# Performance work log

Measured on AMD Instinct MI355X. Metric: run time of the kernel, lower is better.

## Reference

```python
import jax, jax.numpy as jnp
import numpy as np

D_IN, H, H1, H2 = 50, 64, 32, 1

def setup_inputs() -> dict:
    key = jax.random.key(0)
    ks = jax.random.split(key, 13)
    s = 1.0 / np.sqrt(H)
    u = lambda k, shp: jax.random.uniform(k, shp, jnp.float32, -s, s)
    x = jax.random.normal(ks[0], (512, 2048, D_IN), jnp.float32)
    return {
        "x": x,
        "W_ih0": u(ks[1], (H, D_IN)), "W_hh0": u(ks[2], (H, H)),
        "b_ih0": u(ks[3], (H,)),      "b_hh0": u(ks[4], (H,)),
        "W_ih1": u(ks[5], (H, H)),    "W_hh1": u(ks[6], (H, H)),
        "b_ih1": u(ks[7], (H,)),      "b_hh1": u(ks[8], (H,)),
        "W1": u(ks[9], (H1, H)),      "b1": u(ks[10], (H1,)),
        "W2": u(ks[11], (H2, H1)),    "b2": u(ks[12], (H2,)),
    }

def reference(x, W_ih0, W_hh0, b_ih0, b_hh0, W_ih1, W_hh1, b_ih1, b_hh1, W1, b1, W2, b2):
    B = x.shape[0]
    # Precompute input projections for layer 0 for all timesteps: [S, B, H]
    xt = jnp.swapaxes(x, 0, 1)  # [S, B, D_IN]
    x_proj0 = jnp.einsum('sbd,hd->sbh', xt, W_ih0) + b_ih0 + b_hh0

    h0 = jnp.zeros((B, H), x.dtype)

    def step(carry, xp):
        h1, h2 = carry
        h1 = jnp.tanh(xp + h1 @ W_hh0.T)
        h2 = jnp.tanh(h1 @ W_ih1.T + b_ih1 + h2 @ W_hh1.T + b_hh1)
        return (h1, h2), None

    (h1f, h2f), _ = jax.lax.scan(step, (h0, h0), x_proj0)
    hidden = jax.nn.relu(h2f @ W1.T + b1)
    return jax.nn.sigmoid(hidden @ W2.T + b2)
```

## Files before the change

### kernel.cpp

```cpp
#include <hip/hip_runtime.h>

#define S_LEN 2048
#define DIN   50
#define H     64

__device__ __forceinline__ float tanh_fast(float v) {
    float e = __builtin_amdgcn_exp2f(v * 2.885390082f);
    return 1.0f - 2.0f * __builtin_amdgcn_rcpf(e + 1.0f);
}

__device__ __forceinline__ float sum4groups(float v) {
#if __has_builtin(__builtin_amdgcn_permlane16_swap) && __has_builtin(__builtin_amdgcn_permlane32_swap)
    typedef unsigned u2 __attribute__((ext_vector_type(2)));
    u2 r = __builtin_amdgcn_permlane16_swap(__float_as_uint(v), __float_as_uint(v), false, false);
    float s = __uint_as_float(r[0]) + __uint_as_float(r[1]);
    u2 t = __builtin_amdgcn_permlane32_swap(__float_as_uint(s), __float_as_uint(s), false, false);
    return __uint_as_float(t[0]) + __uint_as_float(t[1]);
#else
    v += __shfl_xor(v, 16, 64);
    v += __shfl_xor(v, 32, 64);
    return v;
#endif
}

__global__ __launch_bounds__(256)
__attribute__((amdgpu_waves_per_eu(2, 2)))
void rnn_fused(const float* __restrict__ x,
               const float* __restrict__ W_ih0, const float* __restrict__ W_hh0,
               const float* __restrict__ b_ih0, const float* __restrict__ b_hh0,
               const float* __restrict__ W_ih1, const float* __restrict__ W_hh1,
               const float* __restrict__ b_ih1, const float* __restrict__ b_hh1,
               const float* __restrict__ W1, const float* __restrict__ b1,
               const float* __restrict__ W2, const float* __restrict__ b2,
               float* __restrict__ out)
{
    const int b    = blockIdx.x;
    const int tid  = threadIdx.x;
    const int lane = tid & 63;
    const int w    = tid >> 6;
    const int j    = lane & 15;
    const int kg   = lane >> 4;
    const int outj = 16 * w + j;

    __shared__ __align__(16) float xs[2][4][16];
    __shared__ __align__(16) float h1s[H];
    __shared__ __align__(16) float h2s[H];

    float wx[13];
    #pragma unroll
    for (int i = 0; i < 13; ++i) {
        int c = 13 * kg + i;
        wx[i] = (c < DIN) ? W_ih0[outj * DIN + c] : 0.0f;
    }
    float whh0_l[16], wih1_l[16], whh1_l[16];
    #pragma unroll
    for (int i = 0; i < 16; ++i) {
        whh0_l[i] = W_hh0[outj * H + 16 * kg + i];
        wih1_l[i] = W_ih1[outj * H + 16 * kg + i];
        whh1_l[i] = W_hh1[outj * H + 16 * kg + i];
    }
    const float bias0 = b_ih0[outj] + b_hh0[outj];
    const float bias1 = b_ih1[outj] + b_hh1[outj];

    const float* __restrict__ xrow = x + (size_t)b * (size_t)(S_LEN * DIN);

    const int  sw   = tid >> 4, sj = tid & 15;
    const int  scol = 13 * sw + sj;
    const bool sval = (tid < 64) && (sj < 13) && (scol < DIN);

    if (tid < 64) xs[0][sw][sj] = sval ? xrow[scol] : 0.0f;
    float pfA = sval ? xrow[1 * DIN + scol] : 0.0f;
    float pfB = sval ? xrow[2 * DIN + scol] : 0.0f;
    const float* xpf = xrow + 3 * DIN + scol;

    float h1c[16], h2c[16];
    #pragma unroll
    for (int i = 0; i < 16; ++i) { h1c[i] = 0.0f; h2c[i] = 0.0f; }

    __syncthreads();

    float xacc;
    {
        float a0 = 0, a1 = 0, a2 = 0, a3 = 0;
        #pragma unroll
        for (int q = 0; q < 3; ++q) {
            float4 xv = *(const float4*)&xs[0][kg][4 * q];
            a0 = fmaf(xv.x, wx[4 * q + 0], a0);
            a1 = fmaf(xv.y, wx[4 * q + 1], a1);
            a2 = fmaf(xv.z, wx[4 * q + 2], a2);
            a3 = fmaf(xv.w, wx[4 * q + 3], a3);
        }
        a0 = fmaf(xs[0][kg][12], wx[12], a0);
        xacc = (a0 + a1) + (a2 + a3);
    }

#define STEP_BODY(CUR, NXT, PFOK)                                              \
    {                                                                          \
                  \
        float a0 = xacc, a1 = 0, a2 = 0, a3 = 0;                               \
        _Pragma("unroll")                                                      \
        for (int q = 0; q < 4; ++q) {                                          \
            a0 = fmaf(h1c[4 * q + 0], whh0_l[4 * q + 0], a0);                  \
            a1 = fmaf(h1c[4 * q + 1], whh0_l[4 * q + 1], a1);                  \
            a2 = fmaf(h1c[4 * q + 2], whh0_l[4 * q + 2], a2);                  \
            a3 = fmaf(h1c[4 * q + 3], whh0_l[4 * q + 3], a3);                  \
        }                                                                      \
        float h1n = tanh_fast(sum4groups((a0 + a1) + (a2 + a3)) + bias0);      \
                               \
        if (tid < 64) xs[NXT][sw][sj] = pfA;                                   \
        pfA = pfB;                                                             \
        pfB = (sval && (PFOK)) ? *xpf : 0.0f;                                  \
        xpf += DIN;                                                            \
                          \
        float c0 = 0, c1 = 0, c2 = 0, c3 = 0;                                  \
        _Pragma("unroll")                                                      \
        for (int q = 0; q < 4; ++q) {                                          \
            c0 = fmaf(h2c[4 * q + 0], whh1_l[4 * q + 0], c0);                  \
            c1 = fmaf(h2c[4 * q + 1], whh1_l[4 * q + 1], c1);                  \
            c2 = fmaf(h2c[4 * q + 2], whh1_l[4 * q + 2], c2);                  \
            c3 = fmaf(h2c[4 * q + 3], whh1_l[4 * q + 3], c3);                  \
        }                                                                      \
        if (kg == 0) h1s[16 * w + j] = h1n;                                    \
        __syncthreads();                    \
                    \
        _Pragma("unroll")                                                      \
        for (int q = 0; q < 4; ++q)                                            \
            *(float4*)&h1c[4 * q] = *(const float4*)&h1s[16 * kg + 4 * q];     \
                \
        float xn0 = 0, xn1 = 0, xn2 = 0, xn3 = 0;                              \
        _Pragma("unroll")                                                      \
        for (int q = 0; q < 3; ++q) {                                          \
            float4 xv = *(const float4*)&xs[NXT][kg][4 * q];                   \
            xn0 = fmaf(xv.x, wx[4 * q + 0], xn0);                              \
            xn1 = fmaf(xv.y, wx[4 * q + 1], xn1);                              \
            xn2 = fmaf(xv.z, wx[4 * q + 2], xn2);                              \
            xn3 = fmaf(xv.w, wx[4 * q + 3], xn3);                              \
        }                                                                      \
        xn0 = fmaf(xs[NXT][kg][12], wx[12], xn0);                              \
                                            \
        _Pragma("unroll")                                                      \
        for (int q = 0; q < 4; ++q) {                                          \
            c0 = fmaf(h1c[4 * q + 0], wih1_l[4 * q + 0], c0);                  \
            c1 = fmaf(h1c[4 * q + 1], wih1_l[4 * q + 1], c1);                  \
            c2 = fmaf(h1c[4 * q + 2], wih1_l[4 * q + 2], c2);                  \
            c3 = fmaf(h1c[4 * q + 3], wih1_l[4 * q + 3], c3);                  \
        }                                                                      \
        float h2n = tanh_fast(sum4groups((c0 + c1) + (c2 + c3)) + bias1);      \
        if (kg == 0) h2s[16 * w + j] = h2n;                                    \
        __syncthreads();                               \
        _Pragma("unroll")                                                      \
        for (int q = 0; q < 4; ++q)                                            \
            *(float4*)&h2c[4 * q] = *(const float4*)&h2s[16 * kg + 4 * q];     \
        xacc = (xn0 + xn1) + (xn2 + xn3);                                      \
    }

    for (int s = 0; s < S_LEN; s += 2) {
        STEP_BODY(0, 1, s + 3 < S_LEN)
        STEP_BODY(1, 0, s + 4 < S_LEN)
    }
#undef STEP_BODY

    if (tid < 64) {
        float hv = 0.0f;
        if (lane < 32) {
            float acc = b1[lane];
            #pragma unroll
            for (int k = 0; k < H; ++k)
                acc = fmaf(h2s[k], W1[lane * H + k], acc);
            hv = fmaxf(acc, 0.0f) * W2[lane];
        }
        #pragma unroll
        for (int off = 32; off; off >>= 1)
            hv += __shfl_xor(hv, off, 64);
        if (lane == 0)
            out[b] = 1.0f / (1.0f + __expf(-(hv + b2[0])));
    }
}

extern "C" void kernel_launch(void* const* d_in, const int* in_sizes, int n_in,
                              void* d_out, int out_size, void* d_ws, size_t ws_size,
                              hipStream_t stream) {
    const float* x     = (const float*)d_in[0];
    const float* W_ih0 = (const float*)d_in[1];
    const float* W_hh0 = (const float*)d_in[2];
    const float* b_ih0 = (const float*)d_in[3];
    const float* b_hh0 = (const float*)d_in[4];
    const float* W_ih1 = (const float*)d_in[5];
    const float* W_hh1 = (const float*)d_in[6];
    const float* b_ih1 = (const float*)d_in[7];
    const float* b_hh1 = (const float*)d_in[8];
    const float* W1    = (const float*)d_in[9];
    const float* b1    = (const float*)d_in[10];
    const float* W2    = (const float*)d_in[11];
    const float* b2    = (const float*)d_in[12];
    float* out = (float*)d_out;

    rnn_fused<<<dim3(512), dim3(256), 0, stream>>>(
        x, W_ih0, W_hh0, b_ih0, b_hh0,
        W_ih1, W_hh1, b_ih1, b_hh1,
        W1, b1, W2, b2, out);
}
```

Baseline: 1.064 ms.

## Split each RNN block over eight waves with an eight-way reduction

Doubles the threads per sequence block from 256 to 512, so each wave owns 8 hidden units instead of 16. The reduction dimension is now split into 8 lane groups of 8 elements, so each thread holds half as many weights and does half as many FMAs per step. A DPP row-rotate add is added in front of the existing permlane reduction. The intent is to shorten per-thread work on the serial recurrence and raise wave occupancy, at the cost of an extra reduction stage and barriers that must synchronise twice as many waves every timestep.

```diff
diff --git a/kernel.cpp b/kernel.cpp
--- a/kernel.cpp
+++ b/kernel.cpp
@@ -9,13 +9,20 @@
     return 1.0f - 2.0f * __builtin_amdgcn_rcpf(e + 1.0f);
 }
 
-__device__ __forceinline__ float sum4groups(float v) {
+__device__ __forceinline__ float red8(float v) {
+#if __has_builtin(__builtin_amdgcn_update_dpp)
+    float t = __uint_as_float((unsigned)__builtin_amdgcn_update_dpp(
+        0, (int)__float_as_uint(v), 0x128 , 0xF, 0xF, true));
+    v += t;
+#else
+    v += __shfl_xor(v, 8, 64);
+#endif
 #if __has_builtin(__builtin_amdgcn_permlane16_swap) && __has_builtin(__builtin_amdgcn_permlane32_swap)
     typedef unsigned u2 __attribute__((ext_vector_type(2)));
     u2 r = __builtin_amdgcn_permlane16_swap(__float_as_uint(v), __float_as_uint(v), false, false);
     float s = __uint_as_float(r[0]) + __uint_as_float(r[1]);
-    u2 t = __builtin_amdgcn_permlane32_swap(__float_as_uint(s), __float_as_uint(s), false, false);
-    return __uint_as_float(t[0]) + __uint_as_float(t[1]);
+    u2 q = __builtin_amdgcn_permlane32_swap(__float_as_uint(s), __float_as_uint(s), false, false);
+    return __uint_as_float(q[0]) + __uint_as_float(q[1]);
 #else
     v += __shfl_xor(v, 16, 64);
     v += __shfl_xor(v, 32, 64);
@@ -23,8 +30,8 @@
 #endif
 }
 
-__global__ __launch_bounds__(256)
-__attribute__((amdgpu_waves_per_eu(2, 2)))
+__global__ __launch_bounds__(512)
+__attribute__((amdgpu_waves_per_eu(4, 4)))
 void rnn_fused(const float* __restrict__ x,
                const float* __restrict__ W_ih0, const float* __restrict__ W_hh0,
                const float* __restrict__ b_ih0, const float* __restrict__ b_hh0,
@@ -38,120 +45,105 @@
     const int tid  = threadIdx.x;
     const int lane = tid & 63;
     const int w    = tid >> 6;
-    const int j    = lane & 15;
-    const int kg   = lane >> 4;
-    const int outj = 16 * w + j;
+    const int j    = lane & 7;
+    const int kg   = lane >> 3;
+    const int outj = 8 * w + j;
 
-    __shared__ __align__(16) float xs[2][4][16];
+    __shared__ __align__(16) float xs[2][8][8];
     __shared__ __align__(16) float h1s[H];
     __shared__ __align__(16) float h2s[H];
 
-    float wx[13];
+    float wx[7];
     #pragma unroll
-    for (int i = 0; i < 13; ++i) {
-        int c = 13 * kg + i;
+    for (int i = 0; i < 7; ++i) {
+        int c = 7 * kg + i;
         wx[i] = (c < DIN) ? W_ih0[outj * DIN + c] : 0.0f;
     }
-    float whh0_l[16], wih1_l[16], whh1_l[16];
+    float whh0_l[8], wih1_l[8], whh1_l[8];
     #pragma unroll
-    for (int i = 0; i < 16; ++i) {
-        whh0_l[i] = W_hh0[outj * H + 16 * kg + i];
-        wih1_l[i] = W_ih1[outj * H + 16 * kg + i];
-        whh1_l[i] = W_hh1[outj * H + 16 * kg + i];
+    for (int i = 0; i < 8; ++i) {
+        whh0_l[i] = W_hh0[outj * H + 8 * kg + i];
+        wih1_l[i] = W_ih1[outj * H + 8 * kg + i];
+        whh1_l[i] = W_hh1[outj * H + 8 * kg + i];
     }
     const float bias0 = b_ih0[outj] + b_hh0[outj];
     const float bias1 = b_ih1[outj] + b_hh1[outj];
 
     const float* __restrict__ xrow = x + (size_t)b * (size_t)(S_LEN * DIN);
 
-    const int  sw   = tid >> 4, sj = tid & 15;
-    const int  scol = 13 * sw + sj;
-    const bool sval = (tid < 64) && (sj < 13) && (scol < DIN);
+    const int  sw   = lane >> 3, sj = lane & 7;
+    const int  scol = 7 * sw + sj;
+    const bool sval = (tid < 64) && (sj < 7) && (scol < DIN);
 
     if (tid < 64) xs[0][sw][sj] = sval ? xrow[scol] : 0.0f;
     float pfA = sval ? xrow[1 * DIN + scol] : 0.0f;
     float pfB = sval ? xrow[2 * DIN + scol] : 0.0f;
     const float* xpf = xrow + 3 * DIN + scol;
 
-    float h1c[16], h2c[16];
+    float h1c[8], h2c[8];
     #pragma unroll
-    for (int i = 0; i < 16; ++i) { h1c[i] = 0.0f; h2c[i] = 0.0f; }
+    for (int i = 0; i < 8; ++i) { h1c[i] = 0.0f; h2c[i] = 0.0f; }
 
     __syncthreads();
 
     float xacc;
     {
-        float a0 = 0, a1 = 0, a2 = 0, a3 = 0;
-        #pragma unroll
-        for (int q = 0; q < 3; ++q) {
-            float4 xv = *(const float4*)&xs[0][kg][4 * q];
-            a0 = fmaf(xv.x, wx[4 * q + 0], a0);
-            a1 = fmaf(xv.y, wx[4 * q + 1], a1);
-            a2 = fmaf(xv.z, wx[4 * q + 2], a2);
-            a3 = fmaf(xv.w, wx[4 * q + 3], a3);
-        }
-        a0 = fmaf(xs[0][kg][12], wx[12], a0);
-        xacc = (a0 + a1) + (a2 + a3);
+        float4 xv0 = *(const float4*)&xs[0][kg][0];
+        float4 xv1 = *(const float4*)&xs[0][kg][4];
+        float a0 = xv0.x * wx[0], a1 = xv0.y * wx[1];
+        a0 = fmaf(xv0.z, wx[2], a0);  a1 = fmaf(xv0.w, wx[3], a1);
+        a0 = fmaf(xv1.x, wx[4], a0);  a1 = fmaf(xv1.y, wx[5], a1);
+        a0 = fmaf(xv1.z, wx[6], a0);
+        xacc = a0 + a1;
     }
 
 #define STEP_BODY(CUR, NXT, PFOK)                                              \
     {                                                                          \
                   \
-        float a0 = xacc, a1 = 0, a2 = 0, a3 = 0;                               \
+        float a0 = xacc, a1 = 0.0f;                                            \
         _Pragma("unroll")                                                      \
         for (int q = 0; q < 4; ++q) {                                          \
-            a0 = fmaf(h1c[4 * q + 0], whh0_l[4 * q + 0], a0);                  \
-            a1 = fmaf(h1c[4 * q + 1], whh0_l[4 * q + 1], a1);                  \
-            a2 = fmaf(h1c[4 * q + 2], whh0_l[4 * q + 2], a2);                  \
-            a3 = fmaf(h1c[4 * q + 3], whh0_l[4 * q + 3], a3);                  \
+            a0 = fmaf(h1c[2 * q + 0], whh0_l[2 * q + 0], a0);                  \
+            a1 = fmaf(h1c[2 * q + 1], whh0_l[2 * q + 1], a1);                  \
         }                                                                      \
-        float h1n = tanh_fast(sum4groups((a0 + a1) + (a2 + a3)) + bias0);      \
+        float h1n = tanh_fast(red8(a0 + a1) + bias0);                          \
                                \
         if (tid < 64) xs[NXT][sw][sj] = pfA;                                   \
         pfA = pfB;                                                             \
         pfB = (sval && (PFOK)) ? *xpf : 0.0f;                                  \
         xpf += DIN;                                                            \
-                          \
-        float c0 = 0, c1 = 0, c2 = 0, c3 = 0;                                  \
+                               \
+        float c0 = 0.0f, c1 = 0.0f;                                            \
         _Pragma("unroll")                                                      \
         for (int q = 0; q < 4; ++q) {                                          \
-            c0 = fmaf(h2c[4 * q + 0], whh1_l[4 * q + 0], c0);                  \
-            c1 = fmaf(h2c[4 * q + 1], whh1_l[4 * q + 1], c1);                  \
-            c2 = fmaf(h2c[4 * q + 2], whh1_l[4 * q + 2], c2);                  \
-            c3 = fmaf(h2c[4 * q + 3], whh1_l[4 * q + 3], c3);                  \
+            c0 = fmaf(h2c[2 * q + 0], whh1_l[2 * q + 0], c0);                  \
+            c1 = fmaf(h2c[2 * q + 1], whh1_l[2 * q + 1], c1);                  \
         }                                                                      \
-        if (kg == 0) h1s[16 * w + j] = h1n;                                    \
+        if (kg == 0) h1s[8 * w + j] = h1n;                                     \
         __syncthreads();                    \
-                    \
-        _Pragma("unroll")                                                      \
-        for (int q = 0; q < 4; ++q)                                            \
-            *(float4*)&h1c[4 * q] = *(const float4*)&h1s[16 * kg + 4 * q];     \
+                                                 \
+        *(float4*)&h1c[0] = *(const float4*)&h1s[8 * kg + 0];                  \
+        *(float4*)&h1c[4] = *(const float4*)&h1s[8 * kg + 4];                  \
                 \
-        float xn0 = 0, xn1 = 0, xn2 = 0, xn3 = 0;                              \
-        _Pragma("unroll")                                                      \
-        for (int q = 0; q < 3; ++q) {                                          \
-            float4 xv = *(const float4*)&xs[NXT][kg][4 * q];                   \
-            xn0 = fmaf(xv.x, wx[4 * q + 0], xn0);                              \
-            xn1 = fmaf(xv.y, wx[4 * q + 1], xn1);                              \
-            xn2 = fmaf(xv.z, wx[4 * q + 2], xn2);                              \
-            xn3 = fmaf(xv.w, wx[4 * q + 3], xn3);                              \
-        }                                                                      \
-        xn0 = fmaf(xs[NXT][kg][12], wx[12], xn0);                              \
-                                            \
+        float4 xv0 = *(const float4*)&xs[NXT][kg][0];                          \
+        float4 xv1 = *(const float4*)&xs[NXT][kg][4];                          \
+        float xn0 = xv0.x * wx[0], xn1 = xv0.y * wx[1];                        \
+        xn0 = fmaf(xv0.z, wx[2], xn0);  xn1 = fmaf(xv0.w, wx[3], xn1);         \
+        xn0 = fmaf(xv1.x, wx[4], xn0);  xn1 = fmaf(xv1.y, wx[5], xn1);         \
+        xn0 = fmaf(xv1.z, wx[6], xn0);                                         \
+                                          \
+        float c2 = 0.0f, c3 = 0.0f;                                            \
         _Pragma("unroll")                                                      \
         for (int q = 0; q < 4; ++q) {                                          \
-            c0 = fmaf(h1c[4 * q + 0], wih1_l[4 * q + 0], c0);                  \
-            c1 = fmaf(h1c[4 * q + 1], wih1_l[4 * q + 1], c1);                  \
-            c2 = fmaf(h1c[4 * q + 2], wih1_l[4 * q + 2], c2);                  \
-            c3 = fmaf(h1c[4 * q + 3], wih1_l[4 * q + 3], c3);                  \
+            c2 = fmaf(h1c[2 * q + 0], wih1_l[2 * q + 0], c2);                  \
+            c3 = fmaf(h1c[2 * q + 1], wih1_l[2 * q + 1], c3);                  \
         }                                                                      \
-        float h2n = tanh_fast(sum4groups((c0 + c1) + (c2 + c3)) + bias1);      \
-        if (kg == 0) h2s[16 * w + j] = h2n;                                    \
+        float h2n = tanh_fast(red8((c0 + c2) + (c1 + c3)) + bias1);            \
+        if (kg == 0) h2s[8 * w + j] = h2n;                                     \
         __syncthreads();                               \
-        _Pragma("unroll")                                                      \
-        for (int q = 0; q < 4; ++q)                                            \
-            *(float4*)&h2c[4 * q] = *(const float4*)&h2s[16 * kg + 4 * q];     \
-        xacc = (xn0 + xn1) + (xn2 + xn3);                                      \
+        *(float4*)&h2c[0] = *(const float4*)&h2s[8 * kg + 0];                  \
+        *(float4*)&h2c[4] = *(const float4*)&h2s[8 * kg + 4];                  \
+        xacc = xn0 + xn1;                                                      \
     }
 
     for (int s = 0; s < S_LEN; s += 2) {
@@ -195,7 +187,7 @@
     const float* b2    = (const float*)d_in[12];
     float* out = (float*)d_out;
 
-    rnn_fused<<<dim3(512), dim3(256), 0, stream>>>(
+    rnn_fused<<<dim3(512), dim3(512), 0, stream>>>(
         x, W_ih0, W_hh0, b_ih0, b_hh0,
         W_ih1, W_hh1, b_ih1, b_hh1,
         W1, b1, W2, b2, out);
```

After: 1.084 ms. Within noise of the previous version (+1.9%).

## Skew layer recurrences into one barrier per step and batch input projections per chunk

Applied to the files above, without the earlier changes.

Restructures the time loop so that each interval computes layer-1 step t and layer-0 step t+1 together from double-buffered shared hidden states. This halves the barriers per timestep, from two to one. The layer-0 input projection is no longer done incrementally every step; it is precomputed for 32-step chunks, staging raw x in shared memory and giving each wave full 50-wide weight rows. The cost is a periodic refill phase with extra barriers and more registers (50 input weights per thread), which could hurt occupancy.

```diff
diff --git a/kernel.cpp b/kernel.cpp
--- a/kernel.cpp
+++ b/kernel.cpp
@@ -3,19 +3,23 @@
 #define S_LEN 2048
 #define DIN   50
 #define H     64
+#define XB    32
+#define XPROWS (XB + 1)
+#define XRPAD  52
+#define XRAWN  (XPROWS * XRPAD)
 
 __device__ __forceinline__ float tanh_fast(float v) {
     float e = __builtin_amdgcn_exp2f(v * 2.885390082f);
     return 1.0f - 2.0f * __builtin_amdgcn_rcpf(e + 1.0f);
 }
 
-__device__ __forceinline__ float sum4groups(float v) {
+__device__ __forceinline__ float red4(float v) {
 #if __has_builtin(__builtin_amdgcn_permlane16_swap) && __has_builtin(__builtin_amdgcn_permlane32_swap)
     typedef unsigned u2 __attribute__((ext_vector_type(2)));
     u2 r = __builtin_amdgcn_permlane16_swap(__float_as_uint(v), __float_as_uint(v), false, false);
     float s = __uint_as_float(r[0]) + __uint_as_float(r[1]);
-    u2 t = __builtin_amdgcn_permlane32_swap(__float_as_uint(s), __float_as_uint(s), false, false);
-    return __uint_as_float(t[0]) + __uint_as_float(t[1]);
+    u2 q = __builtin_amdgcn_permlane32_swap(__float_as_uint(s), __float_as_uint(s), false, false);
+    return __uint_as_float(q[0]) + __uint_as_float(q[1]);
 #else
     v += __shfl_xor(v, 16, 64);
     v += __shfl_xor(v, 32, 64);
@@ -42,16 +46,16 @@
     const int kg   = lane >> 4;
     const int outj = 16 * w + j;
 
-    __shared__ __align__(16) float xs[2][4][16];
-    __shared__ __align__(16) float h1s[H];
-    __shared__ __align__(16) float h2s[H];
-
-    float wx[13];
+    __shared__ __align__(16) float xraw[XRAWN];
+    __shared__ __align__(16) float xp[XPROWS][H];
+    __shared__ __align__(16) float h1s[2][H];
+    __shared__ __align__(16) float h2s[2][H];
+
+    float wxf[DIN];
     #pragma unroll
-    for (int i = 0; i < 13; ++i) {
-        int c = 13 * kg + i;
-        wx[i] = (c < DIN) ? W_ih0[outj * DIN + c] : 0.0f;
-    }
+    for (int d = 0; d < DIN; ++d) wxf[d] = W_ih0[lane * DIN + d];
+    const float bias0 = b_ih0[lane] + b_hh0[lane];
+
     float whh0_l[16], wih1_l[16], whh1_l[16];
     #pragma unroll
     for (int i = 0; i < 16; ++i) {
@@ -59,45 +63,88 @@
         wih1_l[i] = W_ih1[outj * H + 16 * kg + i];
         whh1_l[i] = W_hh1[outj * H + 16 * kg + i];
     }
-    const float bias0 = b_ih0[outj] + b_hh0[outj];
     const float bias1 = b_ih1[outj] + b_hh1[outj];
 
     const float* __restrict__ xrow = x + (size_t)b * (size_t)(S_LEN * DIN);
 
-    const int  sw   = tid >> 4, sj = tid & 15;
-    const int  scol = 13 * sw + sj;
-    const bool sval = (tid < 64) && (sj < 13) && (scol < DIN);
-
-    if (tid < 64) xs[0][sw][sj] = sval ? xrow[scol] : 0.0f;
-    float pfA = sval ? xrow[1 * DIN + scol] : 0.0f;
-    float pfB = sval ? xrow[2 * DIN + scol] : 0.0f;
-    const float* xpf = xrow + 3 * DIN + scol;
+    auto refill = [&](int T) {
+        #pragma unroll
+        for (int r = 0; r < 7; ++r) {
+            int f = tid + 256 * r;
+            if (f < XRAWN) {
+                int row = f / XRPAD;
+                int col = f - row * XRPAD;
+                int t   = T + row;
+                float v = 0.0f;
+                if (col < DIN && t < S_LEN) v = xrow[(size_t)t * DIN + col];
+                xraw[f] = v;
+            }
+        }
+        __syncthreads();
+        #pragma unroll
+        for (int r = 0; r < 9; ++r) {
+            int u = w + 4 * r;
+            if (u < XPROWS) {
+                const float4* xr4 = (const float4*)&xraw[u * XRPAD];
+                float a0 = bias0, a1 = 0.0f;
+                #pragma unroll
+                for (int q = 0; q < 12; ++q) {
+                    float4 v = xr4[q];
+                    a0 = fmaf(v.x, wxf[4 * q + 0], a0);
+                    a1 = fmaf(v.y, wxf[4 * q + 1], a1);
+                    a0 = fmaf(v.z, wxf[4 * q + 2], a0);
+                    a1 = fmaf(v.w, wxf[4 * q + 3], a1);
+                }
+                float2 vt = *(const float2*)&xraw[u * XRPAD + 48];
+                a0 = fmaf(vt.x, wxf[48], a0);
+                a1 = fmaf(vt.y, wxf[49], a1);
+                xp[u][lane] = a0 + a1;
+            }
+        }
+        __syncthreads();
+    };
 
     float h1c[16], h2c[16];
-    #pragma unroll
-    for (int i = 0; i < 16; ++i) { h1c[i] = 0.0f; h2c[i] = 0.0f; }
-
+    const float* xpp0 = &xp[0][outj];
+
+    refill(0);
+    {
+        float h1n = tanh_fast(xpp0[0]);
+        if (kg == 0) h1s[0][outj] = h1n;
+        if (tid < 64) h2s[1][lane] = 0.0f;
+    }
     __syncthreads();
 
-    float xacc;
-    {
-        float a0 = 0, a1 = 0, a2 = 0, a3 = 0;
-        #pragma unroll
-        for (int q = 0; q < 3; ++q) {
-            float4 xv = *(const float4*)&xs[0][kg][4 * q];
-            a0 = fmaf(xv.x, wx[4 * q + 0], a0);
-            a1 = fmaf(xv.y, wx[4 * q + 1], a1);
-            a2 = fmaf(xv.z, wx[4 * q + 2], a2);
-            a3 = fmaf(xv.w, wx[4 * q + 3], a3);
-        }
-        a0 = fmaf(xs[0][kg][12], wx[12], a0);
-        xacc = (a0 + a1) + (a2 + a3);
-    }
-
-#define STEP_BODY(CUR, NXT, PFOK)                                              \
+#define INTERVAL(PAR, NPAR, XPIDX)                                             \
     {                                                                          \
-                  \
-        float a0 = xacc, a1 = 0, a2 = 0, a3 = 0;                               \
+        *(float4*)&h1c[0]  = *(const float4*)&h1s[PAR][16 * kg + 0];           \
+        *(float4*)&h1c[4]  = *(const float4*)&h1s[PAR][16 * kg + 4];           \
+        *(float4*)&h1c[8]  = *(const float4*)&h1s[PAR][16 * kg + 8];           \
+        *(float4*)&h1c[12] = *(const float4*)&h1s[PAR][16 * kg + 12];          \
+        *(float4*)&h2c[0]  = *(const float4*)&h2s[NPAR][16 * kg + 0];          \
+        *(float4*)&h2c[4]  = *(const float4*)&h2s[NPAR][16 * kg + 4];          \
+        *(float4*)&h2c[8]  = *(const float4*)&h2s[NPAR][16 * kg + 8];          \
+        *(float4*)&h2c[12] = *(const float4*)&h2s[NPAR][16 * kg + 12];         \
+        float xpn = xpp0[(XPIDX) * H];                                         \
+                 \
+        float c0 = 0, c1 = 0, c2 = 0, c3 = 0;                                  \
+        _Pragma("unroll")                                                      \
+        for (int q = 0; q < 4; ++q) {                                          \
+            c0 = fmaf(h1c[4 * q + 0], wih1_l[4 * q + 0], c0);                  \
+            c1 = fmaf(h1c[4 * q + 1], wih1_l[4 * q + 1], c1);                  \
+            c2 = fmaf(h1c[4 * q + 2], wih1_l[4 * q + 2], c2);                  \
+            c3 = fmaf(h1c[4 * q + 3], wih1_l[4 * q + 3], c3);                  \
+        }                                                                      \
+        _Pragma("unroll")                                                      \
+        for (int q = 0; q < 4; ++q) {                                          \
+            c0 = fmaf(h2c[4 * q + 0], whh1_l[4 * q + 0], c0);                  \
+            c1 = fmaf(h2c[4 * q + 1], whh1_l[4 * q + 1], c1);                  \
+            c2 = fmaf(h2c[4 * q + 2], whh1_l[4 * q + 2], c2);                  \
+            c3 = fmaf(h2c[4 * q + 3], whh1_l[4 * q + 3], c3);                  \
+        }                                                                      \
+        float h2n = tanh_fast(red4((c0 + c1) + (c2 + c3)) + bias1);            \
+                            \
+        float a0 = 0, a1 = 0, a2 = 0, a3 = 0;                                  \
         _Pragma("unroll")                                                      \
         for (int q = 0; q < 4; ++q) {                                          \
             a0 = fmaf(h1c[4 * q + 0], whh0_l[4 * q + 0], a0);                  \
@@ -105,60 +152,23 @@
             a2 = fmaf(h1c[4 * q + 2], whh0_l[4 * q + 2], a2);                  \
             a3 = fmaf(h1c[4 * q + 3], whh0_l[4 * q + 3], a3);                  \
         }                                                                      \
-        float h1n = tanh_fast(sum4groups((a0 + a1) + (a2 + a3)) + bias0);      \
-                               \
-        if (tid < 64) xs[NXT][sw][sj] = pfA;                                   \
-        pfA = pfB;                                                             \
-        pfB = (sval && (PFOK)) ? *xpf : 0.0f;                                  \
-        xpf += DIN;                                                            \
-                          \
-        float c0 = 0, c1 = 0, c2 = 0, c3 = 0;                                  \
-        _Pragma("unroll")                                                      \
-        for (int q = 0; q < 4; ++q) {                                          \
-            c0 = fmaf(h2c[4 * q + 0], whh1_l[4 * q + 0], c0);                  \
-            c1 = fmaf(h2c[4 * q + 1], whh1_l[4 * q + 1], c1);                  \
-            c2 = fmaf(h2c[4 * q + 2], whh1_l[4 * q + 2], c2);                  \
-            c3 = fmaf(h2c[4 * q + 3], whh1_l[4 * q + 3], c3);                  \
-        }                                                                      \
-        if (kg == 0) h1s[16 * w + j] = h1n;                                    \
-        __syncthreads();                    \
-                    \
-        _Pragma("unroll")                                                      \
-        for (int q = 0; q < 4; ++q)                                            \
-            *(float4*)&h1c[4 * q] = *(const float4*)&h1s[16 * kg + 4 * q];     \
-                \
-        float xn0 = 0, xn1 = 0, xn2 = 0, xn3 = 0;                              \
-        _Pragma("unroll")                                                      \
-        for (int q = 0; q < 3; ++q) {                                          \
-            float4 xv = *(const float4*)&xs[NXT][kg][4 * q];                   \
-            xn0 = fmaf(xv.x, wx[4 * q + 0], xn0);                              \
-            xn1 = fmaf(xv.y, wx[4 * q + 1], xn1);                              \
-            xn2 = fmaf(xv.z, wx[4 * q + 2], xn2);                              \
-            xn3 = fmaf(xv.w, wx[4 * q + 3], xn3);                              \
-        }                                                                      \
-        xn0 = fmaf(xs[NXT][kg][12], wx[12], xn0);                              \
-                                            \
-        _Pragma("unroll")                                                      \
-        for (int q = 0; q < 4; ++q) {                                          \
-            c0 = fmaf(h1c[4 * q + 0], wih1_l[4 * q + 0], c0);                  \
-            c1 = fmaf(h1c[4 * q + 1], wih1_l[4 * q + 1], c1);                  \
-            c2 = fmaf(h1c[4 * q + 2], wih1_l[4 * q + 2], c2);                  \
-            c3 = fmaf(h1c[4 * q + 3], wih1_l[4 * q + 3], c3);                  \
-        }                                                                      \
-        float h2n = tanh_fast(sum4groups((c0 + c1) + (c2 + c3)) + bias1);      \
-        if (kg == 0) h2s[16 * w + j] = h2n;                                    \
-        __syncthreads();                               \
-        _Pragma("unroll")                                                      \
-        for (int q = 0; q < 4; ++q)                                            \
-            *(float4*)&h2c[4 * q] = *(const float4*)&h2s[16 * kg + 4 * q];     \
-        xacc = (xn0 + xn1) + (xn2 + xn3);                                      \
-    }
-
-    for (int s = 0; s < S_LEN; s += 2) {
-        STEP_BODY(0, 1, s + 3 < S_LEN)
-        STEP_BODY(1, 0, s + 4 < S_LEN)
-    }
-#undef STEP_BODY
+        float h1n = tanh_fast(red4((a0 + a1) + (a2 + a3)) + xpn);              \
+        if (kg == 0) {                                                         \
+            h2s[PAR][outj]  = h2n;                                             \
+            h1s[NPAR][outj] = h1n;                                             \
+        }                                                                      \
+        __syncthreads();                                                       \
+    }
+
+    for (int T = 0; T < S_LEN; T += XB) {
+        if (T) refill(T);
+        #pragma unroll
+        for (int ui = 0; ui < XB; ui += 2) {
+            INTERVAL(0, 1, ui + 1)
+            INTERVAL(1, 0, ui + 2)
+        }
+    }
+#undef INTERVAL
 
     if (tid < 64) {
         float hv = 0.0f;
@@ -166,7 +176,7 @@
             float acc = b1[lane];
             #pragma unroll
             for (int k = 0; k < H; ++k)
-                acc = fmaf(h2s[k], W1[lane * H + k], acc);
+                acc = fmaf(h2s[1][k], W1[lane * H + k], acc);
             hv = fmaxf(acc, 0.0f) * W2[lane];
         }
         #pragma unroll
```

New measurement: 993.0 us. -6.7%, faster.
